# Kernel optimization log

Measured on AMD Instinct MI355X. Metric: run time of the kernel, lower is better.

The kernel has to match this reference:

```python
import jax, jax.numpy as jnp
import numpy as np

B, N, IN_DIM, DIM = 16, 512, 2048, 512
K, DEPTH, HEADS, DH, MLP, NC = 4, 2, 8, 64, 512, 10
INNER = HEADS * DH  # 512
TOPK = 2
TEMP = 1.0


def setup_inputs() -> dict:
    key = jax.random.key(0)
    ks = jax.random.split(key, 16)
    g = lambda i, shape, s=0.02: jax.random.normal(ks[i], shape, dtype=jnp.float32) * s
    z = lambda shape: jnp.zeros(shape, jnp.float32)
    o = lambda shape: jnp.ones(shape, jnp.float32)
    return {
        "x": jax.random.normal(ks[0], (B, N, IN_DIM), dtype=jnp.float32),
        "proj_w": g(1, (IN_DIM, DIM)),
        "proj_b": z((DIM,)),
        "qkv_w": g(2, (K, DEPTH, DIM, 3 * INNER)),
        "ao_w": g(3, (K, DEPTH, INNER, DIM)),
        "ao_b": z((K, DEPTH, DIM)),
        "ln1_g": o((K, DEPTH, DIM)),
        "ln1_b": z((K, DEPTH, DIM)),
        "ln2_g": o((K, DEPTH, DIM)),
        "ln2_b": z((K, DEPTH, DIM)),
        "mlp_w1": g(4, (K, DEPTH, DIM, MLP)),
        "mlp_b1": z((K, DEPTH, MLP)),
        "mlp_w2": g(5, (K, DEPTH, MLP, DIM)),
        "mlp_b2": z((K, DEPTH, DIM)),
        "lnf_g": o((K, DIM)),
        "lnf_b": z((K, DIM)),
        "router_w1": g(6, (DIM, 256)),
        "router_b1": z((256,)),
        "router_w2": g(7, (256, K)),
        "router_b2": z((K,)),
        "head_w1": g(8, (DIM, 128)),
        "head_b1": z((128,)),
        "head_w2": g(9, (128, NC)),
        "head_b2": z((NC,)),
    }


def _ln(x, g, b):
    m = x.mean(-1, keepdims=True)
    v = jnp.mean((x - m) ** 2, axis=-1, keepdims=True)
    return (x - m) * jax.lax.rsqrt(v + 1e-5) * g + b


def _expert(h, qkv_w, ao_w, ao_b, ln1g, ln1b, ln2g, ln2b, w1, b1, w2, b2, lnfg, lnfb):
    # h: [B, N, DIM]; pre-norm transformer, depth=DEPTH, then final LN + mean-pool.
    Bb, Nn, _ = h.shape
    scale = DH ** -0.5
    for l in range(DEPTH):
        y = _ln(h, ln1g[l], ln1b[l])
        q, k, v = jnp.split(y @ qkv_w[l], 3, axis=-1)
        q = q.reshape(Bb, Nn, HEADS, DH)
        k = k.reshape(Bb, Nn, HEADS, DH)
        v = v.reshape(Bb, Nn, HEADS, DH)
        att = jax.nn.softmax(jnp.einsum('bqhd,bkhd->bhqk', q, k) * scale, axis=-1)
        o = jnp.einsum('bhqk,bkhd->bqhd', att, v).reshape(Bb, Nn, INNER)
        h = h + o @ ao_w[l] + ao_b[l]
        y2 = _ln(h, ln2g[l], ln2b[l])
        h = h + jax.nn.gelu(y2 @ w1[l] + b1[l]) @ w2[l] + b2[l]
    return _ln(h, lnfg, lnfb).mean(1)  # [B, DIM]


def reference(x, proj_w, proj_b, qkv_w, ao_w, ao_b, ln1_g, ln1_b, ln2_g, ln2_b,
              mlp_w1, mlp_b1, mlp_w2, mlp_b2, lnf_g, lnf_b,
              router_w1, router_b1, router_w2, router_b2,
              head_w1, head_b1, head_w2, head_b2):
    # Shared projection (mode='shared')
    H = x @ proj_w + proj_b                       # [B, N, DIM]
    bag = H.mean(1)                               # [B, DIM]
    rl = jax.nn.relu(bag @ router_w1 + router_b1) @ router_w2 + router_b2
    g_soft = jax.nn.softmax(rl / TEMP, axis=-1)   # [B, K]
    vals, idx = jax.lax.top_k(g_soft, TOPK)
    w = vals / (vals.sum(-1, keepdims=True) + 1e-8)
    # Dense combine weights: [B, K], zero for non-selected experts.
    Wfull = (jax.nn.one_hot(idx, K, dtype=H.dtype) * w[..., None]).sum(1)
    latents = jnp.stack([
        _expert(H, qkv_w[e], ao_w[e], ao_b[e], ln1_g[e], ln1_b[e], ln2_g[e], ln2_b[e],
                mlp_w1[e], mlp_b1[e], mlp_w2[e], mlp_b2[e], lnf_g[e], lnf_b[e])
        for e in range(K)
    ])                                            # [K, B, DIM]
    z = jnp.einsum('kbd,bk->bd', latents, Wfull)  # weighted combine
    logits = jax.nn.relu(z @ head_w1 + head_b1) @ head_w2 + head_b2
    return (z, logits, g_soft)
```

## Files before the change

kernel.cpp:

```cpp
#include <hip/hip_runtime.h>
#include <math.h>

typedef unsigned short u16;
typedef unsigned int u32;
typedef float f32x4 __attribute__((ext_vector_type(4)));
typedef unsigned short u16x8 __attribute__((ext_vector_type(8)));
typedef unsigned short u16x4 __attribute__((ext_vector_type(4)));
typedef _Float16 f16x8 __attribute__((ext_vector_type(8)));
typedef _Float16 f16x4 __attribute__((ext_vector_type(4)));

#define DEV static __device__ __forceinline__

constexpr int BB = 16, NN = 512, DIM = 512, DEP = 2;
constexpr long ROWS = (long)BB * NN;

DEV u16 f2h(float f){ _Float16 h = (_Float16)f; return __builtin_bit_cast(u16, h); }
DEV float h2f(u16 u){ return (float)__builtin_bit_cast(_Float16, u); }
DEV f32x4 mfma16h(u16x8 a, u16x8 b, f32x4 c){
  return __builtin_amdgcn_mfma_f32_16x16x32_f16(__builtin_bit_cast(f16x8, a), __builtin_bit_cast(f16x8, b), c, 0, 0, 0);
}
DEV u32 pkrtz(float a, float b){ auto r = __builtin_amdgcn_cvt_pkrtz(a, b); return __builtin_bit_cast(u32, r); }
DEV u16x4 cvt4(f32x4 a){ f16x4 h = {(_Float16)a[0], (_Float16)a[1], (_Float16)a[2], (_Float16)a[3]}; return __builtin_bit_cast(u16x4, h); }
DEV float gelu_f(float x){ return 0.5f * x * (1.f + tanhf(0.79788456080286536f * (x + 0.044715f * x * x * x))); }

DEV void gload16(const u16* g, u16* l){
  __builtin_amdgcn_global_load_lds((const __attribute__((address_space(1))) unsigned int*)(const void*)g,
                                   (__attribute__((address_space(3))) unsigned int*)(void*)l, 16, 0, 0);
}

DEV f32x4 vaddv(f32x4 a, f32x4 b){ f32x4 r; r[0]=a[0]+b[0]; r[1]=a[1]+b[1]; r[2]=a[2]+b[2]; r[3]=a[3]+b[3]; return r; }
DEV f32x4 shfl4(f32x4 v, int m){ f32x4 r; r[0]=__shfl_xor(v[0],m); r[1]=__shfl_xor(v[1],m); r[2]=__shfl_xor(v[2],m); r[3]=__shfl_xor(v[3],m); return r; }

__global__ __launch_bounds__(256) void castAll(const float* __restrict__ qkv_w, const float* __restrict__ ao_w,
                                               const float* __restrict__ mlp_w1, const float* __restrict__ mlp_w2,
                                               u16* __restrict__ WQ, u16* __restrict__ WAO,
                                               u16* __restrict__ W1t, u16* __restrict__ W2t)
{
  const int z = blockIdx.z;
  const float* src; u16* dst; int Nd;
  if (z < 8){ src = qkv_w + (long)z * 512 * 1536; dst = WQ + (long)z * 512 * 1536; Nd = 1536; }
  else {
    int m = (z - 8) >> 3, zz = (z - 8) & 7;
    src = (m == 0 ? ao_w : m == 1 ? mlp_w1 : mlp_w2) + (long)zz * 512 * 512;
    dst = (m == 0 ? WAO : m == 1 ? W1t : W2t) + (long)zz * 512 * 512;
    Nd = 512;
  }
  const int n0 = blockIdx.y * 32;
  if (n0 >= Nd) return;
  const int k0 = blockIdx.x * 32;
  __shared__ float t[32][33];
  const int r = threadIdx.x >> 5, cc = threadIdx.x & 31;
  #pragma unroll
  for (int i = 0; i < 4; i++) t[r + i * 8][cc] = src[(long)(k0 + r + i * 8) * Nd + n0 + cc];
  __syncthreads();
  #pragma unroll
  for (int i = 0; i < 4; i++) dst[(long)(n0 + r + i * 8) * 512 + k0 + cc] = f2h(t[cc][r + i * 8]);
}

__global__ __launch_bounds__(256) void castTp(const float* __restrict__ src, u16* __restrict__ dst)
{
  __shared__ float t[32][33];
  const int k0 = blockIdx.x * 32, n0 = blockIdx.y * 32;
  const int r = threadIdx.x >> 5, cc = threadIdx.x & 31;
  #pragma unroll
  for (int i = 0; i < 4; i++) t[r + i * 8][cc] = src[(long)(k0 + r + i * 8) * 512 + n0 + cc];
  __syncthreads();
  #pragma unroll
  for (int i = 0; i < 4; i++) dst[(long)(n0 + r + i * 8) * 2048 + k0 + cc] = f2h(t[cc][r + i * 8]);
}

__global__ __launch_bounds__(256) void xcast(const float* __restrict__ X, u16* __restrict__ Xf)
{
  long i0 = ((long)blockIdx.x * 256 + threadIdx.x) * 8;
  f32x4 v0 = *(const f32x4*)(X + i0), v1 = *(const f32x4*)(X + i0 + 4);
  u16x8 hh;
  hh[0] = f2h(v0[0]); hh[1] = f2h(v0[1]); hh[2] = f2h(v0[2]); hh[3] = f2h(v0[3]);
  hh[4] = f2h(v1[0]); hh[5] = f2h(v1[1]); hh[6] = f2h(v1[2]); hh[7] = f2h(v1[3]);
  *(u16x8*)(Xf + i0) = hh;
}

__global__ __launch_bounds__(256) void gemm_proj(const u16* __restrict__ Xf, const u16* __restrict__ WP,
                                                 const float* __restrict__ bias, u16* __restrict__ Hout)
{
  const int mt = blockIdx.x, nt = blockIdx.y;
  __shared__ __align__(16) u16 As[64 * 64], Bs[128 * 64];
  const int tid = threadIdx.x, lane = tid & 63, wv = tid >> 6;
  const int wm = wv >> 1, wn = wv & 1, l4 = lane >> 4, l15 = lane & 15;
  const long a0 = (long)(mt * 64) * 2048, b0 = (long)(nt * 128) * 2048;
  const int srow = tid >> 3, sslot = tid & 7;
  f32x4 zero = {0.f, 0.f, 0.f, 0.f};
  f32x4 acc[2][4];
  #pragma unroll
  for (int mi = 0; mi < 2; mi++)
    #pragma unroll
    for (int ni = 0; ni < 4; ni++) acc[mi][ni] = zero;

  for (int kt = 0; kt < 2048; kt += 64){
    #pragma unroll
    for (int p = 0; p < 2; p++){
      int r = p * 32 + srow;
      int sg = sslot ^ (r & 7);
      gload16(Xf + a0 + (long)r * 2048 + kt + sg * 8, As + p * 2048 + wv * 512);
    }
    #pragma unroll
    for (int p = 0; p < 4; p++){
      int r = p * 32 + srow;
      int sg = sslot ^ (r & 7);
      gload16(WP + b0 + (long)r * 2048 + kt + sg * 8, Bs + p * 2048 + wv * 512);
    }
    __syncthreads();
    #pragma unroll
    for (int ks = 0; ks < 2; ks++){
      u16x8 af[2], bfr[4];
      #pragma unroll
      for (int mi = 0; mi < 2; mi++){
        int ra = wm * 32 + mi * 16 + l15;
        af[mi] = *(const u16x8*)(As + ra * 64 + ((((ks << 2) | l4)) ^ (ra & 7)) * 8);
      }
      #pragma unroll
      for (int ni = 0; ni < 4; ni++){
        int rb = wn * 64 + ni * 16 + l15;
        bfr[ni] = *(const u16x8*)(Bs + rb * 64 + ((((ks << 2) | l4)) ^ (rb & 7)) * 8);
      }
      #pragma unroll
      for (int mi = 0; mi < 2; mi++)
        #pragma unroll
        for (int ni = 0; ni < 4; ni++)
          acc[mi][ni] = mfma16h(af[mi], bfr[ni], acc[mi][ni]);
    }
    __syncthreads();
  }
  #pragma unroll
  for (int mi = 0; mi < 2; mi++)
    #pragma unroll
    for (int ni = 0; ni < 4; ni++){
      const int gr0 = mt * 64 + wm * 32 + mi * 16 + l4 * 4;
      const int gc = nt * 128 + wn * 64 + ni * 16 + l15;
      float bb = bias[gc];
      #pragma unroll
      for (int i = 0; i < 4; i++) Hout[(long)(gr0 + i) * 512 + gc] = f2h(acc[mi][ni][i] + bb);
    }
}

template<int EPI, int MT>
__global__ __launch_bounds__(256) void gemm_bt(const u16* __restrict__ A, int K, long sAe,
                                               const u16* __restrict__ Bt, long sBe,
                                               const float* __restrict__ bias, int sBiasE,
                                               u16* __restrict__ Cout, long sCe, int N,
                                               const int* __restrict__ pairs,
                                               const u16* __restrict__ resin)
{
  constexpr int MI = MT / 32;
  constexpr int PSH = (MT == 128) ? 2 : 3;
  const int pe = pairs[blockIdx.x >> PSH];
  const int e = pe >> 4, bb = pe & 15;
  const int row0 = bb * 512 + (blockIdx.x & ((1 << PSH) - 1)) * MT;
  const int nt = blockIdx.y;
  A += (long)e * sAe + (long)row0 * K;
  Bt += (long)e * sBe + (long)(nt * 128) * K;
  const float* bias_e = bias ? bias + (long)e * sBiasE : nullptr;

  __shared__ __align__(16) u16 As[MT * 64];
  __shared__ __align__(16) u16 Bs[128 * 64];
  const int tid = threadIdx.x, lane = tid & 63, wv = tid >> 6;
  const int wm = wv >> 1, wn = wv & 1, l4 = lane >> 4, l15 = lane & 15;
  const int srow = tid >> 3, sslot = tid & 7;
  f32x4 zero = {0.f, 0.f, 0.f, 0.f};
  f32x4 acc[MI][4];
  #pragma unroll
  for (int mi = 0; mi < MI; mi++)
    #pragma unroll
    for (int ni = 0; ni < 4; ni++) acc[mi][ni] = zero;

  for (int kt = 0; kt < K; kt += 64){
    #pragma unroll
    for (int p = 0; p < MI; p++){
      int r = p * 32 + srow;
      int sg = sslot ^ (r & 7);
      gload16(A + (long)r * K + kt + sg * 8, As + p * 2048 + wv * 512);
    }
    #pragma unroll
    for (int p = 0; p < 4; p++){
      int r = p * 32 + srow;
      int sg = sslot ^ (r & 7);
      gload16(Bt + (long)r * K + kt + sg * 8, Bs + p * 2048 + wv * 512);
    }
    __syncthreads();
    #pragma unroll
    for (int ks = 0; ks < 2; ks++){
      u16x8 af[MI], bfr[4];
      #pragma unroll
      for (int mi = 0; mi < MI; mi++){
        int ra = wm * (MT / 2) + mi * 16 + l15;
        af[mi] = *(const u16x8*)(As + ra * 64 + ((((ks << 2) | l4)) ^ (ra & 7)) * 8);
      }
      #pragma unroll
      for (int ni = 0; ni < 4; ni++){
        int rb = wn * 64 + ni * 16 + l15;
        bfr[ni] = *(const u16x8*)(Bs + rb * 64 + ((((ks << 2) | l4)) ^ (rb & 7)) * 8);
      }
      #pragma unroll
      for (int mi = 0; mi < MI; mi++)
        #pragma unroll
        for (int ni = 0; ni < 4; ni++)
          acc[mi][ni] = mfma16h(af[mi], bfr[ni], acc[mi][ni]);
    }
    __syncthreads();
  }

  #pragma unroll
  for (int mi = 0; mi < MI; mi++)
    #pragma unroll
    for (int ni = 0; ni < 4; ni++){
      const int gr0 = row0 + wm * (MT / 2) + mi * 16 + l4 * 4;
      const int gc = nt * 128 + wn * 64 + ni * 16 + l15;
      float bb2 = bias_e ? bias_e[gc] : 0.f;
      #pragma unroll
      for (int i = 0; i < 4; i++){
        float val = acc[mi][ni][i] + bb2;
        long idx = (long)e * sCe + (long)(gr0 + i) * N + gc;
        if (EPI == 0){
          Cout[idx] = f2h(val);
        } else if (EPI == 1){
          Cout[idx] = f2h(gelu_f(val));
        } else if (EPI == 2){
          Cout[idx] = f2h(h2f(Cout[idx]) + val);
        } else {
          Cout[idx] = f2h(h2f(resin[(long)(gr0 + i) * N + gc]) + val);
        }
      }
    }
}

__global__ __launch_bounds__(256) void attn(const u16* __restrict__ qkv, u16* __restrict__ obf, const int* __restrict__ pairs)
{
  const int pe = pairs[blockIdx.x & 31];
  const int e = pe >> 4, b = pe & 15;
  const int hh = (blockIdx.x >> 5) & 7;
  const int qt = blockIdx.x >> 8;
  const u16* base = qkv + ((long)e * ROWS + (long)b * NN) * 1536;

  __shared__ u16 Ks[64 * 72];
  __shared__ u16 Vts[64 * 72];
  __shared__ u16 Ps[4][32 * 72];
  const int tid = threadIdx.x, lane = tid & 63, wv = tid >> 6;
  const int l4 = lane >> 4, l15 = lane & 15;
  const int qr0 = qt * 128 + wv * 32;
  constexpr float CSC = 0.125f * 1.44269504088896340736f;

  u16x8 qf[2][2];
  #pragma unroll
  for (int mi = 0; mi < 2; mi++)
    #pragma unroll
    for (int ks = 0; ks < 2; ks++){
      u16x8 raw = *(const u16x8*)(base + (long)(qr0 + mi * 16 + l15) * 1536 + hh * 64 + ks * 32 + l4 * 8);
      #pragma unroll
      for (int j = 0; j < 8; j++) qf[mi][ks][j] = f2h(h2f(raw[j]) * CSC);
    }

  f32x4 zero = {0.f, 0.f, 0.f, 0.f};
  f32x4 o[2][4]; float lrun[2] = {0.f, 0.f};
  #pragma unroll
  for (int mi = 0; mi < 2; mi++)
    #pragma unroll
    for (int df = 0; df < 4; df++) o[mi][df] = zero;
  const int sr = tid >> 3, ss = tid & 7;

  for (int c = 0; c < 8; c++){
    const int kk0 = c * 64;
    u16x8 kv0 = *(const u16x8*)(base + (long)(kk0 + sr) * 1536 + 512 + hh * 64 + ss * 8);
    u16x8 kv1 = *(const u16x8*)(base + (long)(kk0 + sr + 32) * 1536 + 512 + hh * 64 + ss * 8);
    u16x8 vv0 = *(const u16x8*)(base + (long)(kk0 + sr) * 1536 + 1024 + hh * 64 + ss * 8);
    u16x8 vv1 = *(const u16x8*)(base + (long)(kk0 + sr + 32) * 1536 + 1024 + hh * 64 + ss * 8);
    __syncthreads();
    *(u16x8*)(Ks + sr * 72 + ss * 8) = kv0;
    *(u16x8*)(Ks + (sr + 32) * 72 + ss * 8) = kv1;
    #pragma unroll
    for (int j = 0; j < 8; j++){
      int d = ss * 8 + j;
      Vts[d * 72 + (sr ^ (ss * 8))] = vv0[j];
      Vts[d * 72 + ((sr + 32) ^ (ss * 8))] = vv1[j];
    }
    __syncthreads();

    u16x8 kf[4][2];
    #pragma unroll
    for (int n = 0; n < 4; n++)
      #pragma unroll
      for (int ks = 0; ks < 2; ks++)
        kf[n][ks] = *(const u16x8*)(Ks + (n * 16 + l15) * 72 + ks * 32 + l4 * 8);

    f32x4 sv[2][4];
    __builtin_amdgcn_s_setprio(1);
    #pragma unroll
    for (int mi = 0; mi < 2; mi++)
      #pragma unroll
      for (int n = 0; n < 4; n++){
        sv[mi][n] = zero;
        sv[mi][n] = mfma16h(kf[n][0], qf[mi][0], sv[mi][n]);
        sv[mi][n] = mfma16h(kf[n][1], qf[mi][1], sv[mi][n]);
      }
    __builtin_amdgcn_s_setprio(0);

    #pragma unroll
    for (int mi = 0; mi < 2; mi++){
      float lp = 0.f;
      #pragma unroll
      for (int n = 0; n < 4; n++){
        float p0 = __builtin_amdgcn_exp2f(sv[mi][n][0]);
        float p1 = __builtin_amdgcn_exp2f(sv[mi][n][1]);
        float p2 = __builtin_amdgcn_exp2f(sv[mi][n][2]);
        float p3 = __builtin_amdgcn_exp2f(sv[mi][n][3]);
        lp += (p0 + p1) + (p2 + p3);
        union { u32 w[2]; u16x4 h; } pk;
        pk.w[0] = pkrtz(p0, p1);
        pk.w[1] = pkrtz(p2, p3);
        *(u16x4*)(&Ps[wv][(mi * 16 + l15) * 72 + n * 16 + l4 * 4]) = pk.h;
      }
      lp += __shfl_xor(lp, 16);
      lp += __shfl_xor(lp, 32);
      lrun[mi] += lp;
    }

    u16x8 pf[2][2], vf[4][2];
    #pragma unroll
    for (int mi = 0; mi < 2; mi++)
      #pragma unroll
      for (int k2 = 0; k2 < 2; k2++)
        pf[mi][k2] = *(const u16x8*)(&Ps[wv][(mi * 16 + l15) * 72 + k2 * 32 + l4 * 8]);
    #pragma unroll
    for (int df = 0; df < 4; df++)
      #pragma unroll
      for (int k2 = 0; k2 < 2; k2++){
        int d = df * 16 + l15;
        int swz = ((d >> 3) & 7) * 8;
        vf[df][k2] = *(const u16x8*)(Vts + d * 72 + ((k2 * 32 + l4 * 8) ^ swz));
      }
    __builtin_amdgcn_s_setprio(1);
    #pragma unroll
    for (int mi = 0; mi < 2; mi++)
      #pragma unroll
      for (int df = 0; df < 4; df++){
        o[mi][df] = mfma16h(vf[df][0], pf[mi][0], o[mi][df]);
        o[mi][df] = mfma16h(vf[df][1], pf[mi][1], o[mi][df]);
      }
    __builtin_amdgcn_s_setprio(0);
  }

  #pragma unroll
  for (int mi = 0; mi < 2; mi++){
    float inv = 1.f / lrun[mi];
    long rb = (long)e * ROWS * DIM + (long)(b * NN + qr0 + mi * 16 + l15) * DIM + hh * 64;
    #pragma unroll
    for (int df = 0; df < 4; df++){
      f32x4 a;
      #pragma unroll
      for (int i = 0; i < 4; i++) a[i] = o[mi][df][i] * inv;
      *(u16x4*)(obf + rb + df * 16 + l4 * 4) = cvt4(a);
    }
  }
}

__global__ __launch_bounds__(256) void ln_rows(const u16* __restrict__ hin, long sHe,
                                               const float* __restrict__ g, const float* __restrict__ bta,
                                               int sGE, u16* __restrict__ outb, const int* __restrict__ pairs)
{
  const int pe = pairs[blockIdx.x >> 7];
  const int e = pe >> 4;
  const int tid = threadIdx.x, lane = tid & 63, wv = tid >> 6;
  const int row = (pe & 15) * 512 + ((blockIdx.x & 127) << 2) + wv;
  const u16* x = hin + (long)e * sHe + (long)row * DIM + lane * 8;
  u16x8 vh = *(const u16x8*)x;
  float v[8];
  #pragma unroll
  for (int j = 0; j < 8; j++) v[j] = h2f(vh[j]);
  float s = 0.f, sq = 0.f;
  #pragma unroll
  for (int j = 0; j < 8; j++){ s += v[j]; sq += v[j] * v[j]; }
  #pragma unroll
  for (int m = 32; m >= 1; m >>= 1){ s += __shfl_xor(s, m); sq += __shfl_xor(sq, m); }
  float mean = s * (1.f / DIM); float var = sq * (1.f / DIM) - mean * mean;
  float inv = rsqrtf(var + 1e-5f);
  const float* ge = g + (long)e * sGE + lane * 8;
  const float* be = bta + (long)e * sGE + lane * 8;
  f32x4 g0 = *(const f32x4*)ge, g1 = *(const f32x4*)(ge + 4);
  f32x4 b0 = *(const f32x4*)be, b1 = *(const f32x4*)(be + 4);
  u16x8 yo;
  #pragma unroll
  for (int j = 0; j < 4; j++) yo[j] = f2h((v[j] - mean) * inv * g0[j] + b0[j]);
  #pragma unroll
  for (int j = 0; j < 4; j++) yo[4 + j] = f2h((v[4 + j] - mean) * inv * g1[j] + b1[j]);
  *(u16x8*)(outb + ((long)e * ROWS + row) * DIM + lane * 8) = yo;
}

__global__ __launch_bounds__(512) void bag_partial(const u16* __restrict__ H, float* __restrict__ bagp)
{
  const int b = blockIdx.x, c = blockIdx.y;
  const int tid = threadIdx.x;
  const u16* r = H + ((long)b * 512 + c * 64) * DIM + tid;
  float s = 0.f;
  #pragma unroll 8
  for (int n = 0; n < 64; n++) s += h2f(r[n * DIM]);
  bagp[((long)c * BB + b) * DIM + tid] = s;
}

__global__ __launch_bounds__(256) void router_mm(const float* __restrict__ bagp, const float* __restrict__ rw1,
                                                 float* __restrict__ hidp)
{
  const int kc = blockIdx.x, b = blockIdx.y;
  const int tid = threadIdx.x;
  __shared__ float bs[64];
  if (tid < 64){
    int k = kc * 64 + tid;
    float s = 0.f;
    #pragma unroll
    for (int c = 0; c < 8; c++) s += bagp[((long)c * BB + b) * DIM + k];
    bs[tid] = s * (1.f / NN);
  }
  __syncthreads();
  float a = 0.f;
  #pragma unroll 8
  for (int k = 0; k < 64; k++) a += bs[k] * rw1[(long)(kc * 64 + k) * 256 + tid];
  hidp[((long)b * 8 + kc) * 256 + tid] = a;
}

__global__ __launch_bounds__(256) void router_fin(const float* __restrict__ hidp,
                                                  const float* __restrict__ rb1,
                                                  const float* __restrict__ rw2, const float* __restrict__ rb2,
                                                  float* __restrict__ gout, float* __restrict__ wexp, int* __restrict__ pairs)
{
  const int b = blockIdx.x;
  const int tid = threadIdx.x, lane = tid & 63, wv = tid >> 6;
  __shared__ f32x4 red2[4];
  float a = rb1[tid];
  #pragma unroll
  for (int kc = 0; kc < 8; kc++) a += hidp[((long)b * 8 + kc) * 256 + tid];
  float h = fmaxf(a, 0.f);
  f32x4 w4 = *(const f32x4*)(rw2 + tid * 4);
  f32x4 s = {h * w4[0], h * w4[1], h * w4[2], h * w4[3]};
  s = vaddv(s, shfl4(s, 1)); s = vaddv(s, shfl4(s, 2)); s = vaddv(s, shfl4(s, 4));
  s = vaddv(s, shfl4(s, 8)); s = vaddv(s, shfl4(s, 16)); s = vaddv(s, shfl4(s, 32));
  if (lane == 0) red2[wv] = s;
  __syncthreads();
  if (tid == 0){
    f32x4 lg = vaddv(vaddv(red2[0], red2[1]), vaddv(red2[2], red2[3]));
    float l4a[4]; float m = -3e38f;
    #pragma unroll
    for (int k = 0; k < 4; k++){ l4a[k] = lg[k] + rb2[k]; m = fmaxf(m, l4a[k]); }
    float ex[4]; float ssum2 = 0;
    #pragma unroll
    for (int k = 0; k < 4; k++){ ex[k] = expf(l4a[k] - m); ssum2 += ex[k]; }
    float gv[4];
    #pragma unroll
    for (int k = 0; k < 4; k++){ gv[k] = ex[k] / ssum2; gout[b * 4 + k] = gv[k]; }
    int i0 = 0; float v0 = gv[0];
    #pragma unroll
    for (int k = 1; k < 4; k++) if (gv[k] > v0){ v0 = gv[k]; i0 = k; }
    int i1 = -1; float v1 = -1.f;
    #pragma unroll
    for (int k = 0; k < 4; k++) if (k != i0 && gv[k] > v1){ v1 = gv[k]; i1 = k; }
    float den = v0 + v1 + 1e-8f;
    #pragma unroll
    for (int k = 0; k < 4; k++) wexp[k * BB + b] = (k == i0) ? (v0 / den) : ((k == i1) ? (v1 / den) : 0.f);
    pairs[2 * b]     = (i0 << 4) | b;
    pairs[2 * b + 1] = (i1 << 4) | b;
  }
}

__global__ __launch_bounds__(512) void lnf_partial(const u16* __restrict__ hin, const float* __restrict__ g,
                                                   const float* __restrict__ bta, float* __restrict__ part,
                                                   const int* __restrict__ pairs)
{
  const int p = blockIdx.x, chunk = blockIdx.y;
  const int pe = pairs[p];
  const int e = pe >> 4, b = pe & 15;
  const int tid = threadIdx.x, lane = tid & 63, wv = tid >> 6;
  __shared__ float gs[512], bsh[512];
  gs[tid] = g[e * DIM + tid]; bsh[tid] = bta[e * DIM + tid];
  __syncthreads();
  float acc[8] = {0, 0, 0, 0, 0, 0, 0, 0};
  #pragma unroll
  for (int i = 0; i < 8; i++){
    int n = chunk * 64 + i * 8 + wv;
    const u16* r = hin + ((long)e * ROWS + (long)b * NN + n) * DIM + lane * 8;
    u16x8 vh = *(const u16x8*)r;
    float v[8];
    #pragma unroll
    for (int j = 0; j < 8; j++) v[j] = h2f(vh[j]);
    float s = 0, sq = 0;
    #pragma unroll
    for (int j = 0; j < 8; j++){ s += v[j]; sq += v[j] * v[j]; }
    #pragma unroll
    for (int m = 32; m >= 1; m >>= 1){ s += __shfl_xor(s, m); sq += __shfl_xor(sq, m); }
    float mean = s * (1.f / DIM), var = sq * (1.f / DIM) - mean * mean, inv = rsqrtf(var + 1e-5f);
    #pragma unroll
    for (int j = 0; j < 8; j++) acc[j] += (v[j] - mean) * inv * gs[lane * 8 + j] + bsh[lane * 8 + j];
  }
  __shared__ float red[8][512];
  #pragma unroll
  for (int j = 0; j < 8; j++) red[wv][lane * 8 + j] = acc[j];
  __syncthreads();
  float ssum = 0;
  #pragma unroll
  for (int w = 0; w < 8; w++) ssum += red[w][tid];
  part[((long)p * 8 + chunk) * 512 + tid] = ssum;
}

__global__ __launch_bounds__(512) void lnf_fin(const float* __restrict__ part, float* __restrict__ latents,
                                               const int* __restrict__ pairs)
{
  const int p = blockIdx.x;
  const int pe = pairs[p];
  const int e = pe >> 4, b = pe & 15;
  const int tid = threadIdx.x;
  float s = 0.f;
  #pragma unroll
  for (int c = 0; c < 8; c++) s += part[((long)p * 8 + c) * 512 + tid];
  latents[((long)e * BB + b) * DIM + tid] = s * (1.f / NN);
}

__global__ __launch_bounds__(128) void head_l1(const float* __restrict__ latents, const float* __restrict__ wexp,
                                               const float* __restrict__ hw1, float* __restrict__ out,
                                               float* __restrict__ hidp2)
{
  const int b = blockIdx.x, kc = blockIdx.y;
  const int tid = threadIdx.x;
  __shared__ float zs[128];
  float wk[4];
  #pragma unroll
  for (int k = 0; k < 4; k++) wk[k] = wexp[k * BB + b];
  int c = kc * 128 + tid;
  float z = 0.f;
  #pragma unroll
  for (int k = 0; k < 4; k++) if (wk[k] != 0.f) z += wk[k] * latents[((long)k * BB + b) * DIM + c];
  zs[tid] = z;
  out[b * 512 + c] = z;
  __syncthreads();
  float a = 0.f;
  #pragma unroll 8
  for (int cc = 0; cc < 128; cc++) a += zs[cc] * hw1[(long)(kc * 128 + cc) * 128 + tid];
  hidp2[((long)b * 4 + kc) * 128 + tid] = a;
}

__global__ __launch_bounds__(128) void head_fin(const float* __restrict__ hidp2, const float* __restrict__ hb1,
                                                const float* __restrict__ hw2, const float* __restrict__ hb2,
                                                float* __restrict__ out)
{
  const int b = blockIdx.x;
  const int tid = threadIdx.x;
  __shared__ float hid[128];
  float h = hb1[tid];
  #pragma unroll
  for (int kc = 0; kc < 4; kc++) h += hidp2[((long)b * 4 + kc) * 128 + tid];
  hid[tid] = fmaxf(h, 0.f);
  __syncthreads();
  if (tid < 10){
    float s = hb2[tid];
    #pragma unroll 16
    for (int j = 0; j < 128; j++) s += hid[j] * hw2[j * 10 + tid];
    out[8192 + b * 10 + tid] = s;
  }
}

extern "C" void kernel_launch(void* const* d_in, const int* in_sizes, int n_in,
                              void* d_out, int out_size, void* d_ws, size_t ws_size,
                              hipStream_t stream)
{
  const float* x      = (const float*)d_in[0];
  const float* proj_w = (const float*)d_in[1];
  const float* proj_b = (const float*)d_in[2];
  const float* qkv_w  = (const float*)d_in[3];
  const float* ao_w   = (const float*)d_in[4];
  const float* ao_b   = (const float*)d_in[5];
  const float* ln1_g  = (const float*)d_in[6];
  const float* ln1_b  = (const float*)d_in[7];
  const float* ln2_g  = (const float*)d_in[8];
  const float* ln2_b  = (const float*)d_in[9];
  const float* mlp_w1 = (const float*)d_in[10];
  const float* mlp_b1 = (const float*)d_in[11];
  const float* mlp_w2 = (const float*)d_in[12];
  const float* mlp_b2 = (const float*)d_in[13];
  const float* lnf_g  = (const float*)d_in[14];
  const float* lnf_b  = (const float*)d_in[15];
  const float* rw1    = (const float*)d_in[16];
  const float* rb1    = (const float*)d_in[17];
  const float* rw2    = (const float*)d_in[18];
  const float* rb2    = (const float*)d_in[19];
  const float* hw1    = (const float*)d_in[20];
  const float* hb1    = (const float*)d_in[21];
  const float* hw2    = (const float*)d_in[22];
  const float* hb2    = (const float*)d_in[23];
  float* out = (float*)d_out;

  char* base = (char*)d_ws; size_t off = 0;
  auto alloc = [&](size_t bytes) -> void* { void* p = base + off; off = (off + bytes + 255) & ~(size_t)255; return p; };

  u16* WQ   = (u16*)alloc((size_t)8 * 1536 * 512 * 2);
  u16* WAO  = (u16*)alloc((size_t)8 * 512 * 512 * 2);
  u16* W1t  = (u16*)alloc((size_t)8 * 512 * 512 * 2);
  u16* W2t  = (u16*)alloc((size_t)8 * 512 * 512 * 2);
  u16* WP   = (u16*)alloc((size_t)512 * 2048 * 2);
  u16* HF   = (u16*)alloc((size_t)ROWS * 512 * 2);
  u16* HH   = (u16*)alloc((size_t)4 * ROWS * 512 * 2);
  u16* YB   = (u16*)alloc((size_t)4 * ROWS * 512 * 2);
  u16* QKVb = (u16*)alloc((size_t)4 * ROWS * 1536 * 2);
  float* WEXP = (float*)alloc(64 * 4);
  int* PAIRS  = (int*)alloc(32 * 4);
  float* LAT  = (float*)alloc(4 * 16 * 512 * 4);
  float* BAGP = (float*)alloc((size_t)8 * 16 * 512 * 4);
  float* HIDP = (float*)alloc((size_t)16 * 8 * 256 * 4);
  float* PART = (float*)alloc((size_t)32 * 8 * 512 * 4);
  float* HIDP2 = (float*)alloc((size_t)16 * 4 * 128 * 4);
  u16* Y2B = QKVb;
  u16* TB  = QKVb + (size_t)4 * ROWS * 512;
  u16* OB  = YB;
  u16* Xf  = QKVb;

  castAll<<<dim3(16, 48, 32), 256, 0, stream>>>(qkv_w, ao_w, mlp_w1, mlp_w2, WQ, WAO, W1t, W2t);
  castTp<<<dim3(64, 16), 256, 0, stream>>>(proj_w, WP);
  xcast<<<8192, 256, 0, stream>>>(x, Xf);

  gemm_proj<<<dim3(128, 4), 256, 0, stream>>>(Xf, WP, proj_b, HF);
  bag_partial<<<dim3(16, 8), 512, 0, stream>>>(HF, BAGP);
  router_mm<<<dim3(8, 16), 256, 0, stream>>>(BAGP, rw1, HIDP);
  router_fin<<<16, 256, 0, stream>>>(HIDP, rb1, rw2, rb2, out + 8192 + 160, WEXP, PAIRS);

  for (int l = 0; l < 2; l++){
    if (l == 0)
      ln_rows<<<4096, 256, 0, stream>>>(HF, 0L, ln1_g, ln1_b, DEP * 512, YB, PAIRS);
    else
      ln_rows<<<4096, 256, 0, stream>>>(HH, ROWS * 512, ln1_g + 512, ln1_b + 512, DEP * 512, YB, PAIRS);
    gemm_bt<0, 128><<<dim3(128, 12), 256, 0, stream>>>(YB, 512, ROWS * 512, WQ + (long)l * 1536 * 512, (long)DEP * 1536 * 512,
                                                       nullptr, 0, QKVb, ROWS * 1536, 1536, PAIRS, nullptr);
    attn<<<1024, 256, 0, stream>>>(QKVb, OB, PAIRS);
    if (l == 0)
      gemm_bt<3, 64><<<dim3(256, 4), 256, 0, stream>>>(OB, 512, ROWS * 512, WAO, (long)DEP * 512 * 512,
                                                       ao_b, DEP * 512, HH, ROWS * 512, 512, PAIRS, HF);
    else
      gemm_bt<2, 64><<<dim3(256, 4), 256, 0, stream>>>(OB, 512, ROWS * 512, WAO + (long)512 * 512, (long)DEP * 512 * 512,
                                                       ao_b + 512, DEP * 512, HH, ROWS * 512, 512, PAIRS, nullptr);
    ln_rows<<<4096, 256, 0, stream>>>(HH, ROWS * 512, ln2_g + l * 512, ln2_b + l * 512, DEP * 512, Y2B, PAIRS);
    gemm_bt<1, 64><<<dim3(256, 4), 256, 0, stream>>>(Y2B, 512, ROWS * 512, W1t + (long)l * 512 * 512, (long)DEP * 512 * 512,
                                                     mlp_b1 + l * 512, DEP * 512, TB, ROWS * 512, 512, PAIRS, nullptr);
    gemm_bt<2, 64><<<dim3(256, 4), 256, 0, stream>>>(TB, 512, ROWS * 512, W2t + (long)l * 512 * 512, (long)DEP * 512 * 512,
                                                     mlp_b2 + l * 512, DEP * 512, HH, ROWS * 512, 512, PAIRS, nullptr);
  }

  lnf_partial<<<dim3(32, 8), 512, 0, stream>>>(HH, lnf_g, lnf_b, PART, PAIRS);
  lnf_fin<<<32, 512, 0, stream>>>(PART, LAT, PAIRS);
  head_l1<<<dim3(16, 4), 128, 0, stream>>>(LAT, WEXP, hw1, out, HIDP2);
  head_fin<<<16, 128, 0, stream>>>(HIDP2, hb1, hw2, hb2, out);
}
```

Baseline: 412.9 us.

## Double-buffer GEMM shared-memory tiles and prefetch attention K/V into registers

Both GEMM kernels (projection and the generic expert GEMM) now keep two shared-memory buffers for the A and B tiles. Each iteration issues the global-to-LDS loads for the next k-tile before computing on the current one, leaving one barrier per iteration instead of two. The attention kernel loads the next K/V chunk into registers right after the LDS write barrier, so global latency hides behind the current chunk's compute. This doubles LDS use per block, which may lower occupancy, and raises register pressure in attention.

```diff
diff --git a/kernel.cpp b/kernel.cpp
--- a/kernel.cpp
+++ b/kernel.cpp
@@ -83,7 +83,7 @@
                                                  const float* __restrict__ bias, u16* __restrict__ Hout)
 {
   const int mt = blockIdx.x, nt = blockIdx.y;
-  __shared__ __align__(16) u16 As[64 * 64], Bs[128 * 64];
+  __shared__ __align__(16) u16 As[2][64 * 64], Bs[2][128 * 64];
   const int tid = threadIdx.x, lane = tid & 63, wv = tid >> 6;
   const int wm = wv >> 1, wn = wv & 1, l4 = lane >> 4, l15 = lane & 15;
   const long a0 = (long)(mt * 64) * 2048, b0 = (long)(nt * 128) * 2048;
@@ -95,32 +95,40 @@
     #pragma unroll
     for (int ni = 0; ni < 4; ni++) acc[mi][ni] = zero;
 
-  for (int kt = 0; kt < 2048; kt += 64){
+  auto stage = [&](int buf, int kt){
     #pragma unroll
     for (int p = 0; p < 2; p++){
       int r = p * 32 + srow;
       int sg = sslot ^ (r & 7);
-      gload16(Xf + a0 + (long)r * 2048 + kt + sg * 8, As + p * 2048 + wv * 512);
+      gload16(Xf + a0 + (long)r * 2048 + kt + sg * 8, As[buf] + p * 2048 + wv * 512);
     }
     #pragma unroll
     for (int p = 0; p < 4; p++){
       int r = p * 32 + srow;
       int sg = sslot ^ (r & 7);
-      gload16(WP + b0 + (long)r * 2048 + kt + sg * 8, Bs + p * 2048 + wv * 512);
-    }
-    __syncthreads();
+      gload16(WP + b0 + (long)r * 2048 + kt + sg * 8, Bs[buf] + p * 2048 + wv * 512);
+    }
+  };
+
+  stage(0, 0);
+  __syncthreads();
+  int cur = 0;
+  for (int kt = 0; kt < 2048; kt += 64){
+    if (kt + 64 < 2048) stage(cur ^ 1, kt + 64);
+    const u16* Ab = As[cur];
+    const u16* Bb = Bs[cur];
     #pragma unroll
     for (int ks = 0; ks < 2; ks++){
       u16x8 af[2], bfr[4];
       #pragma unroll
       for (int mi = 0; mi < 2; mi++){
         int ra = wm * 32 + mi * 16 + l15;
-        af[mi] = *(const u16x8*)(As + ra * 64 + ((((ks << 2) | l4)) ^ (ra & 7)) * 8);
+        af[mi] = *(const u16x8*)(Ab + ra * 64 + ((((ks << 2) | l4)) ^ (ra & 7)) * 8);
       }
       #pragma unroll
       for (int ni = 0; ni < 4; ni++){
         int rb = wn * 64 + ni * 16 + l15;
-        bfr[ni] = *(const u16x8*)(Bs + rb * 64 + ((((ks << 2) | l4)) ^ (rb & 7)) * 8);
+        bfr[ni] = *(const u16x8*)(Bb + rb * 64 + ((((ks << 2) | l4)) ^ (rb & 7)) * 8);
       }
       #pragma unroll
       for (int mi = 0; mi < 2; mi++)
@@ -129,6 +137,7 @@
           acc[mi][ni] = mfma16h(af[mi], bfr[ni], acc[mi][ni]);
     }
     __syncthreads();
+    cur ^= 1;
   }
   #pragma unroll
   for (int mi = 0; mi < 2; mi++)
@@ -160,8 +169,8 @@
   Bt += (long)e * sBe + (long)(nt * 128) * K;
   const float* bias_e = bias ? bias + (long)e * sBiasE : nullptr;
 
-  __shared__ __align__(16) u16 As[MT * 64];
-  __shared__ __align__(16) u16 Bs[128 * 64];
+  __shared__ __align__(16) u16 As[2][MT * 64];
+  __shared__ __align__(16) u16 Bs[2][128 * 64];
   const int tid = threadIdx.x, lane = tid & 63, wv = tid >> 6;
   const int wm = wv >> 1, wn = wv & 1, l4 = lane >> 4, l15 = lane & 15;
   const int srow = tid >> 3, sslot = tid & 7;
@@ -172,32 +181,40 @@
     #pragma unroll
     for (int ni = 0; ni < 4; ni++) acc[mi][ni] = zero;
 
-  for (int kt = 0; kt < K; kt += 64){
+  auto stage = [&](int buf, int kt){
     #pragma unroll
     for (int p = 0; p < MI; p++){
       int r = p * 32 + srow;
       int sg = sslot ^ (r & 7);
-      gload16(A + (long)r * K + kt + sg * 8, As + p * 2048 + wv * 512);
+      gload16(A + (long)r * K + kt + sg * 8, As[buf] + p * 2048 + wv * 512);
     }
     #pragma unroll
     for (int p = 0; p < 4; p++){
       int r = p * 32 + srow;
       int sg = sslot ^ (r & 7);
-      gload16(Bt + (long)r * K + kt + sg * 8, Bs + p * 2048 + wv * 512);
-    }
-    __syncthreads();
+      gload16(Bt + (long)r * K + kt + sg * 8, Bs[buf] + p * 2048 + wv * 512);
+    }
+  };
+
+  stage(0, 0);
+  __syncthreads();
+  int cur = 0;
+  for (int kt = 0; kt < K; kt += 64){
+    if (kt + 64 < K) stage(cur ^ 1, kt + 64);
+    const u16* Ab = As[cur];
+    const u16* Bb = Bs[cur];
     #pragma unroll
     for (int ks = 0; ks < 2; ks++){
       u16x8 af[MI], bfr[4];
       #pragma unroll
       for (int mi = 0; mi < MI; mi++){
         int ra = wm * (MT / 2) + mi * 16 + l15;
-        af[mi] = *(const u16x8*)(As + ra * 64 + ((((ks << 2) | l4)) ^ (ra & 7)) * 8);
+        af[mi] = *(const u16x8*)(Ab + ra * 64 + ((((ks << 2) | l4)) ^ (ra & 7)) * 8);
       }
       #pragma unroll
       for (int ni = 0; ni < 4; ni++){
         int rb = wn * 64 + ni * 16 + l15;
-        bfr[ni] = *(const u16x8*)(Bs + rb * 64 + ((((ks << 2) | l4)) ^ (rb & 7)) * 8);
+        bfr[ni] = *(const u16x8*)(Bb + rb * 64 + ((((ks << 2) | l4)) ^ (rb & 7)) * 8);
       }
       #pragma unroll
       for (int mi = 0; mi < MI; mi++)
@@ -206,6 +223,7 @@
           acc[mi][ni] = mfma16h(af[mi], bfr[ni], acc[mi][ni]);
     }
     __syncthreads();
+    cur ^= 1;
   }
 
   #pragma unroll
@@ -266,12 +284,12 @@
     for (int df = 0; df < 4; df++) o[mi][df] = zero;
   const int sr = tid >> 3, ss = tid & 7;
 
+  u16x8 kv0 = *(const u16x8*)(base + (long)sr * 1536 + 512 + hh * 64 + ss * 8);
+  u16x8 kv1 = *(const u16x8*)(base + (long)(sr + 32) * 1536 + 512 + hh * 64 + ss * 8);
+  u16x8 vv0 = *(const u16x8*)(base + (long)sr * 1536 + 1024 + hh * 64 + ss * 8);
+  u16x8 vv1 = *(const u16x8*)(base + (long)(sr + 32) * 1536 + 1024 + hh * 64 + ss * 8);
+
   for (int c = 0; c < 8; c++){
-    const int kk0 = c * 64;
-    u16x8 kv0 = *(const u16x8*)(base + (long)(kk0 + sr) * 1536 + 512 + hh * 64 + ss * 8);
-    u16x8 kv1 = *(const u16x8*)(base + (long)(kk0 + sr + 32) * 1536 + 512 + hh * 64 + ss * 8);
-    u16x8 vv0 = *(const u16x8*)(base + (long)(kk0 + sr) * 1536 + 1024 + hh * 64 + ss * 8);
-    u16x8 vv1 = *(const u16x8*)(base + (long)(kk0 + sr + 32) * 1536 + 1024 + hh * 64 + ss * 8);
     __syncthreads();
     *(u16x8*)(Ks + sr * 72 + ss * 8) = kv0;
     *(u16x8*)(Ks + (sr + 32) * 72 + ss * 8) = kv1;
@@ -282,6 +300,13 @@
       Vts[d * 72 + ((sr + 32) ^ (ss * 8))] = vv1[j];
     }
     __syncthreads();
+    if (c < 7){
+      const int kk0 = (c + 1) * 64;
+      kv0 = *(const u16x8*)(base + (long)(kk0 + sr) * 1536 + 512 + hh * 64 + ss * 8);
+      kv1 = *(const u16x8*)(base + (long)(kk0 + sr + 32) * 1536 + 512 + hh * 64 + ss * 8);
+      vv0 = *(const u16x8*)(base + (long)(kk0 + sr) * 1536 + 1024 + hh * 64 + ss * 8);
+      vv1 = *(const u16x8*)(base + (long)(kk0 + sr + 32) * 1536 + 1024 + hh * 64 + ss * 8);
+    }
 
     u16x8 kf[4][2];
     #pragma unroll
```

New measurement: 458.4 us. 11.0% more time.
